# Kernel tuning notes

Hardware: AMD Instinct MI355X
Metric: run time of the kernel (lower is better)

## Reference

```python
import jax, jax.numpy as jnp
import numpy as np

D_MODEL = 1024
NHEAD = 16
HEAD_DIM = D_MODEL // NHEAD
B, T = 2, 2048


def setup_inputs() -> dict:
    key = jax.random.key(0)
    ks = jax.random.split(key, 11)
    s = 1.0 / np.sqrt(D_MODEL)
    inp = {
        'q': jax.random.normal(ks[0], (B, T, D_MODEL), jnp.float32),
        'k': jax.random.normal(ks[1], (B, T, D_MODEL), jnp.float32),
        'v': jax.random.normal(ks[2], (B, T, D_MODEL), jnp.float32),
        'Wq': jax.random.normal(ks[3], (D_MODEL, D_MODEL), jnp.float32) * s,
        'bq': jnp.zeros((D_MODEL,), jnp.float32),
        'Wk': jax.random.normal(ks[4], (D_MODEL, D_MODEL), jnp.float32) * s,
        'bk': jnp.zeros((D_MODEL,), jnp.float32),
        'Wv': jax.random.normal(ks[5], (D_MODEL, D_MODEL), jnp.float32) * s,
        'bv': jnp.zeros((D_MODEL,), jnp.float32),
        'Wo': jax.random.normal(ks[6], (D_MODEL, D_MODEL), jnp.float32) * s,
        'bo': jnp.zeros((D_MODEL,), jnp.float32),
    }
    return inp


def reference(q, k, v, Wq, bq, Wk, bk, Wv, bv, Wo, bo):
    scale = np.sqrt(HEAD_DIM).astype(np.float32)
    # projections (torch Linear: x @ W.T + b), split heads -> [B, H, T, Dh]
    def proj(x, W, b):
        y = jnp.einsum('btd,ed->bte', x, W) + b
        return y.reshape(B, T, NHEAD, HEAD_DIM).transpose(0, 2, 1, 3)
    qh = proj(q, Wq, bq)
    kh = proj(k, Wk, bk)
    vh = proj(v, Wv, bv)
    scores = jnp.einsum('bhqd,bhkd->bhqk', qh, kh) / scale  # [B,H,T,T]
    weights = jax.nn.softmax(scores, axis=-1)
    out = jnp.einsum('bhqk,bhkd->bhqd', weights, vh)        # [B,H,T,Dh]
    out = out.transpose(0, 2, 1, 3).reshape(B, T, D_MODEL)
    return jnp.einsum('btd,ed->bte', out, Wo) + bo
```

## Files before the change

### kernel.cpp

```cpp
#include <hip/hip_runtime.h>
#include <cstdint>
#include <cstddef>


#define D_MODEL 1024
#define NHEAD   16
#define HDIM    64
#define BATCH   2
#define SEQ     2048
#define BT      (BATCH * SEQ)

#define QSCALE 0.18033688011112043f

typedef __bf16 bf16;
typedef __bf16 bf16x8 __attribute__((ext_vector_type(8)));
typedef __bf16 bf16x4 __attribute__((ext_vector_type(4)));
typedef float  floatx4 __attribute__((ext_vector_type(4)));
typedef short  short4v __attribute__((ext_vector_type(4)));

#define MFMA16(a, b, c) __builtin_amdgcn_mfma_f32_16x16x32_bf16((a), (b), (c), 0, 0, 0)

__device__ __forceinline__ floatx4 MFMA16B(bf16x4 a, bf16x4 b, floatx4 c) {
  return __builtin_amdgcn_mfma_f32_16x16x16bf16_1k(
      __builtin_bit_cast(short4v, a), __builtin_bit_cast(short4v, b), c, 0, 0, 0);
}

__device__ __forceinline__ float fexp2(float x) {
  return __builtin_amdgcn_exp2f(x);
}

__device__ __forceinline__ void async_cp16(const bf16* g, bf16* l) {
  __builtin_amdgcn_global_load_lds(
      (__attribute__((address_space(1))) void*)(g),
      (__attribute__((address_space(3))) void*)(l), 16, 0, 0);
}

__global__ __launch_bounds__(256) void cvt7(
    const float* __restrict__ s0, const float* __restrict__ s1,
    const float* __restrict__ s2, const float* __restrict__ s3,
    const float* __restrict__ s4, const float* __restrict__ s5,
    const float* __restrict__ s6,
    bf16* __restrict__ d0, bf16* __restrict__ d1, bf16* __restrict__ d2,
    bf16* __restrict__ d3, bf16* __restrict__ d4, bf16* __restrict__ d5,
    bf16* __restrict__ d6)
{
  const float* src; bf16* dst; int n4;
  switch (blockIdx.y) {
    case 0:  src = s0; dst = d0; n4 = (BT * D_MODEL) / 4; break;
    case 1:  src = s1; dst = d1; n4 = (BT * D_MODEL) / 4; break;
    case 2:  src = s2; dst = d2; n4 = (BT * D_MODEL) / 4; break;
    case 3:  src = s3; dst = d3; n4 = (D_MODEL * D_MODEL) / 4; break;
    case 4:  src = s4; dst = d4; n4 = (D_MODEL * D_MODEL) / 4; break;
    case 5:  src = s5; dst = d5; n4 = (D_MODEL * D_MODEL) / 4; break;
    default: src = s6; dst = d6; n4 = (D_MODEL * D_MODEL) / 4; break;
  }
  int stride = gridDim.x * blockDim.x;
  for (int i = blockIdx.x * blockDim.x + threadIdx.x; i < n4; i += stride) {
    float4 f = ((const float4*)src)[i];
    bf16x4 h;
    h[0] = (bf16)f.x; h[1] = (bf16)f.y; h[2] = (bf16)f.z; h[3] = (bf16)f.w;
    ((bf16x4*)dst)[i] = h;
  }
}

__device__ __forceinline__ void gemm128_core(
    const bf16* __restrict__ A, const bf16* __restrict__ W,
    int m0, int n0, bf16* As, bf16* Bs, floatx4 acc[4][4])
{
  const int t = threadIdx.x;
  const int l = t & 63, w = t >> 6;
  const int quad = l >> 4, lr = l & 15;
  const int wm = (w >> 1) * 64, wn = (w & 1) * 64;

  floatx4 z = {0.f, 0.f, 0.f, 0.f};
#pragma unroll
  for (int i = 0; i < 4; i++)
#pragma unroll
    for (int j = 0; j < 4; j++) acc[i][j] = z;

  for (int kt = 0; kt < 1024; kt += 32) {
    __syncthreads();
#pragma unroll
    for (int i = 0; i < 2; i++) {
      int c = i * 256 + t;
      int row = c >> 2, ci = c & 3;
      async_cp16(A + (size_t)(m0 + row) * 1024 + kt + ci * 8,
                 As + (i * 256 + w * 64) * 8);
      async_cp16(W + (size_t)(n0 + row) * 1024 + kt + ci * 8,
                 Bs + (i * 256 + w * 64) * 8);
    }
    __syncthreads();

    bf16x8 af[4], bfr[4];
#pragma unroll
    for (int i = 0; i < 4; i++) {
      af[i]  = *(const bf16x8*)(As + (wm + i * 16 + lr) * 32 + quad * 8);
      bfr[i] = *(const bf16x8*)(Bs + (wn + i * 16 + lr) * 32 + quad * 8);
    }
#pragma unroll
    for (int i = 0; i < 4; i++)
#pragma unroll
      for (int j = 0; j < 4; j++)
        acc[i][j] = MFMA16(af[i], bfr[j], acc[i][j]);
  }
}

__global__ __launch_bounds__(256) void qkv_gemm(
    const bf16* __restrict__ qb, const bf16* __restrict__ kb, const bf16* __restrict__ vb,
    const bf16* __restrict__ wq, const bf16* __restrict__ wk, const bf16* __restrict__ wv,
    const float* __restrict__ biasq, const float* __restrict__ biask, const float* __restrict__ biasv,
    bf16* __restrict__ qh, bf16* __restrict__ kh, bf16* __restrict__ vt)
{
  __shared__ bf16 As[128 * 32];
  __shared__ bf16 Bs[128 * 32];
  const int zid = blockIdx.z;
  const bf16* A = (zid == 0) ? qb : ((zid == 1) ? kb : vb);
  const bf16* W = (zid == 0) ? wq : ((zid == 1) ? wk : wv);
  const float* bias = (zid == 0) ? biasq : ((zid == 1) ? biask : biasv);
  const int m0 = blockIdx.x * 128, n0 = blockIdx.y * 128;

  floatx4 acc[4][4];
  gemm128_core(A, W, m0, n0, As, Bs, acc);

  const int t = threadIdx.x, l = t & 63, w = t >> 6;
  const int quad = l >> 4, lr = l & 15;
  const int wm = (w >> 1) * 64, wn = (w & 1) * 64;
  const float sc = (zid == 0) ? QSCALE : 1.0f;

  if (zid < 2) {
    bf16* out = (zid == 0) ? qh : kh;
#pragma unroll
    for (int i = 0; i < 4; i++) {
      int mbase = m0 + wm + i * 16 + quad * 4;
      int b  = mbase >> 11;
      int tq = mbase & 2047;
#pragma unroll
      for (int j = 0; j < 4; j++) {
        int n = n0 + wn + j * 16 + lr;
        float bv = bias[n];
        int h = n >> 6, dh = n & 63;
        bf16* p = out + ((size_t)((b * NHEAD + h) * SEQ + tq)) * HDIM + dh;
#pragma unroll
        for (int r = 0; r < 4; r++)
          p[(size_t)r * HDIM] = (bf16)((acc[i][j][r] + bv) * sc);
      }
    }
  } else {
#pragma unroll
    for (int i = 0; i < 4; i++) {
      int mbase = m0 + wm + i * 16 + quad * 4;
      int b  = mbase >> 11;
      int tq = mbase & 2047;
#pragma unroll
      for (int j = 0; j < 4; j++) {
        int n = n0 + wn + j * 16 + lr;
        float bv = bias[n];
        int h = n >> 6, dh = n & 63;
        bf16x4 pk;
#pragma unroll
        for (int r = 0; r < 4; r++) pk[r] = (bf16)(acc[i][j][r] + bv);
        *(bf16x4*)(vt + ((size_t)((b * NHEAD + h) * HDIM + dh)) * SEQ + tq) = pk;
      }
    }
  }
}

__global__ __launch_bounds__(512, 4) void attn_fused(
    const bf16* __restrict__ qh, const bf16* __restrict__ kh,
    const bf16* __restrict__ vt, bf16* __restrict__ attn)
{
  __shared__ __align__(16) char smem[65536];

  const int t = threadIdx.x, l = t & 63, w = t >> 6;
  const int quad = l >> 4, lr = l & 15;
  const int bh = blockIdx.y;
  const int qt0 = blockIdx.x * 128;
  const bf16* qg = qh + (size_t)bh * SEQ * HDIM;
  const bf16* kg = kh + (size_t)bh * SEQ * HDIM;
  const bf16* vg = vt + (size_t)bh * HDIM * SEQ;

  int krow0 = (w * 2) * 8 + (l >> 3);
  int krow1 = (w * 2 + 1) * 8 + (l >> 3);
  int kcl0  = (l & 7) ^ (krow0 & 7);
  int kcl1  = (l & 7) ^ (krow1 & 7);
  int vrow0 = (w * 2) * 4 + (l >> 4);
  int vrow1 = (w * 2 + 1) * 4 + (l >> 4);
  int vcl0  = (l & 15) ^ (vrow0 & 15);
  int vcl1  = (l & 15) ^ (vrow1 & 15);
  const bf16* kga = kg + (size_t)krow0 * HDIM + kcl0 * 8;
  const bf16* kgb = kg + (size_t)krow1 * HDIM + kcl1 * 8;
  const bf16* vga = vg + (size_t)vrow0 * SEQ + vcl0 * 8;
  const bf16* vgb = vg + (size_t)vrow1 * SEQ + vcl1 * 8;

  bf16x8 qf[2];
#pragma unroll
  for (int ko = 0; ko < 2; ko++)
    qf[ko] = *(const bf16x8*)(qg + (size_t)(qt0 + w * 16 + lr) * HDIM
                              + ko * 32 + quad * 8);

  floatx4 zz = {0.f, 0.f, 0.f, 0.f};
  floatx4 Oacc[4];
#pragma unroll
  for (int dt = 0; dt < 4; dt++) Oacc[dt] = zz;
  float mrow = -3.0e38f, lrow = 0.f;

  {
    bf16* Kb = (bf16*)smem;
    bf16* Vb = (bf16*)(smem + 16384);
    async_cp16(kga, Kb + (w * 2) * 512);
    async_cp16(kgb, Kb + (w * 2 + 1) * 512);
    async_cp16(vga, Vb + (w * 2) * 512);
    async_cp16(vgb, Vb + (w * 2 + 1) * 512);
  }

  for (int kt = 0; kt < 16; kt++) {
    const int p = kt & 1;
    __syncthreads();
    if (kt + 1 < 16) {
      bf16* Kb = (bf16*)(smem + (1 - p) * 32768);
      bf16* Vb = (bf16*)(smem + (1 - p) * 32768 + 16384);
      int off = (kt + 1) * 128;
      async_cp16(kga + (size_t)off * HDIM, Kb + (w * 2) * 512);
      async_cp16(kgb + (size_t)off * HDIM, Kb + (w * 2 + 1) * 512);
      async_cp16(vga + off, Vb + (w * 2) * 512);
      async_cp16(vgb + off, Vb + (w * 2 + 1) * 512);
    }
    const bf16* Ks  = (const bf16*)(smem + p * 32768);
    const bf16* Vts = (const bf16*)(smem + p * 32768 + 16384);

    floatx4 s[8];
#pragma unroll
    for (int ni = 0; ni < 8; ni++) {
      const bf16* krow = Ks + (ni * 16 + lr) * 64;
      bf16x8 k0 = *(const bf16x8*)(krow + ((quad ^ (lr & 7)) * 8));
      bf16x8 k1 = *(const bf16x8*)(krow + (((quad + 4) ^ (lr & 7)) * 8));
      floatx4 a = zz;
      a = MFMA16(k0, qf[0], a);
      a = MFMA16(k1, qf[1], a);
      s[ni] = a;
    }

    float rmax = s[0][0];
#pragma unroll
    for (int ni = 0; ni < 8; ni++)
#pragma unroll
      for (int r = 0; r < 4; r++) rmax = fmaxf(rmax, s[ni][r]);
    rmax = fmaxf(rmax, __shfl_xor(rmax, 16, 64));
    rmax = fmaxf(rmax, __shfl_xor(rmax, 32, 64));
    float mnew = fmaxf(mrow, rmax);
    float al = fexp2(mrow - mnew);
    mrow = mnew;

    bf16x4 pk[8];
    float rsum = 0.f;
#pragma unroll
    for (int ni = 0; ni < 8; ni++)
#pragma unroll
      for (int r = 0; r < 4; r++) {
        float pv = fexp2(s[ni][r] - mnew);
        rsum += pv;
        pk[ni][r] = (bf16)pv;
      }
    rsum += __shfl_xor(rsum, 16, 64);
    rsum += __shfl_xor(rsum, 32, 64);
    lrow = lrow * al + rsum;
#pragma unroll
    for (int dt = 0; dt < 4; dt++)
#pragma unroll
      for (int r = 0; r < 4; r++) Oacc[dt][r] *= al;

#pragma unroll
    for (int ni = 0; ni < 8; ni++)
#pragma unroll
      for (int dt = 0; dt < 4; dt++) {
        bf16x4 vf = *(const bf16x4*)(Vts + (dt * 16 + lr) * 128
                                     + (((ni * 2 + (quad >> 1)) ^ lr) * 8)
                                     + (quad & 1) * 4);
        Oacc[dt] = MFMA16B(vf, pk[ni], Oacc[dt]);
      }
  }

  float inv = 1.0f / lrow;
  bf16* Ost = (bf16*)smem;
#pragma unroll
  for (int dt = 0; dt < 4; dt++) {
    bf16x4 ov;
#pragma unroll
    for (int r = 0; r < 4; r++) ov[r] = (bf16)(Oacc[dt][r] * inv);
    *(bf16x4*)(Ost + (size_t)(w * 16 + lr) * 72 + dt * 16 + quad * 4) = ov;
  }
  __syncthreads();

  const int b = bh >> 4, h = bh & 15;
#pragma unroll
  for (int i = 0; i < 2; i++) {
    int c = t + 512 * i;
    int row = c >> 3, ci = c & 7;
    *(int4*)(attn + ((size_t)b * SEQ + qt0 + row) * D_MODEL + h * HDIM + ci * 8) =
        *(const int4*)(Ost + row * 72 + ci * 8);
  }
}

__global__ __launch_bounds__(256) void oproj_gemm(
    const bf16* __restrict__ attn, const bf16* __restrict__ wo,
    const float* __restrict__ bo, float* __restrict__ out)
{
  __shared__ bf16 As[64 * 32];
  __shared__ bf16 Bs[64 * 32];
  const int m0 = blockIdx.x * 64, n0 = blockIdx.y * 64;
  const int t = threadIdx.x, l = t & 63, w = t >> 6;
  const int quad = l >> 4, lr = l & 15;
  const int wm = (w >> 1) * 32, wn = (w & 1) * 32;

  floatx4 z = {0.f, 0.f, 0.f, 0.f};
  floatx4 acc[2][2];
#pragma unroll
  for (int i = 0; i < 2; i++)
#pragma unroll
    for (int j = 0; j < 2; j++) acc[i][j] = z;

  for (int kt = 0; kt < 1024; kt += 32) {
    __syncthreads();
    {
      int row = t >> 2, ci = t & 3;
      async_cp16(attn + (size_t)(m0 + row) * 1024 + kt + ci * 8,
                 As + (w * 64) * 8);
      async_cp16(wo + (size_t)(n0 + row) * 1024 + kt + ci * 8,
                 Bs + (w * 64) * 8);
    }
    __syncthreads();

    bf16x8 af[2], bfr[2];
#pragma unroll
    for (int i = 0; i < 2; i++) {
      af[i]  = *(const bf16x8*)(As + (wm + i * 16 + lr) * 32 + quad * 8);
      bfr[i] = *(const bf16x8*)(Bs + (wn + i * 16 + lr) * 32 + quad * 8);
    }
#pragma unroll
    for (int i = 0; i < 2; i++)
#pragma unroll
      for (int j = 0; j < 2; j++)
        acc[i][j] = MFMA16(af[i], bfr[j], acc[i][j]);
  }

#pragma unroll
  for (int i = 0; i < 2; i++) {
    int m = m0 + wm + i * 16 + quad * 4;
#pragma unroll
    for (int j = 0; j < 2; j++) {
      int n = n0 + wn + j * 16 + lr;
      float bv = bo[n];
      float* p = out + (size_t)m * D_MODEL + n;
#pragma unroll
      for (int r = 0; r < 4; r++)
        p[(size_t)r * D_MODEL] = acc[i][j][r] + bv;
    }
  }
}

extern "C" void kernel_launch(void* const* d_in, const int* in_sizes, int n_in,
                              void* d_out, int out_size, void* d_ws, size_t ws_size,
                              hipStream_t stream)
{
  const float* q  = (const float*)d_in[0];
  const float* k  = (const float*)d_in[1];
  const float* v  = (const float*)d_in[2];
  const float* Wq = (const float*)d_in[3];
  const float* bq = (const float*)d_in[4];
  const float* Wk = (const float*)d_in[5];
  const float* bk = (const float*)d_in[6];
  const float* Wv = (const float*)d_in[7];
  const float* bv = (const float*)d_in[8];
  const float* Wo = (const float*)d_in[9];
  const float* bo = (const float*)d_in[10];

  const size_t NQ = (size_t)BT * D_MODEL;
  const size_t NW = (size_t)D_MODEL * D_MODEL;

  bf16* p = (bf16*)d_ws;
  bf16* qb   = p; p += NQ;
  bf16* kb   = p; p += NQ;
  bf16* vb   = p; p += NQ;
  bf16* wqb  = p; p += NW;
  bf16* wkb  = p; p += NW;
  bf16* wvb  = p; p += NW;
  bf16* wob  = p; p += NW;
  bf16* qhp  = p; p += NQ;
  bf16* khp  = p; p += NQ;
  bf16* vtp  = p; p += NQ;
  bf16* attn = p; p += NQ;

  cvt7<<<dim3(1024, 7, 1), 256, 0, stream>>>(q, k, v, Wq, Wk, Wv, Wo,
                                             qb, kb, vb, wqb, wkb, wvb, wob);
  qkv_gemm<<<dim3(32, 8, 3), 256, 0, stream>>>(qb, kb, vb, wqb, wkb, wvb,
                                               bq, bk, bv, qhp, khp, vtp);
  attn_fused<<<dim3(16, 32, 1), 512, 0, stream>>>(qhp, khp, vtp, attn);
  oproj_gemm<<<dim3(64, 16, 1), 256, 0, stream>>>(attn, wob, bo, (float*)d_out);
}
```

Baseline: 230.7 us.

## Process two query groups per wave in attention and skip small max rescales

The attention kernel now uses 4 waves of 256 threads instead of 8. Each wave handles 32 query rows as two 16-row groups, so every K and V fragment read from LDS feeds two MFMAs. This halves LDS traffic per unit of work and doubles per-wave registers. It also adds a lazy-rescale threshold: the running max and accumulators are updated only when some lane's new max exceeds the old by more than 8 (log2 units). This saves exp and multiply work, but the unnormalized values can grow up to 2^8 before rescaling.

```diff
diff --git a/kernel.cpp b/kernel.cpp
--- a/kernel.cpp
+++ b/kernel.cpp
@@ -165,7 +165,7 @@
   }
 }
 
-__global__ __launch_bounds__(512, 4) void attn_fused(
+__global__ __launch_bounds__(256, 2) void attn_fused(
     const bf16* __restrict__ qh, const bf16* __restrict__ kh,
     const bf16* __restrict__ vt, bf16* __restrict__ attn)
 {
@@ -179,122 +179,138 @@
   const bf16* kg = kh + (size_t)bh * SEQ * HDIM;
   const bf16* vg = vt + (size_t)bh * HDIM * SEQ;
 
-  int krow0 = (w * 2) * 8 + (l >> 3);
-  int krow1 = (w * 2 + 1) * 8 + (l >> 3);
-  int kcl0  = (l & 7) ^ (krow0 & 7);
-  int kcl1  = (l & 7) ^ (krow1 & 7);
-  int vrow0 = (w * 2) * 4 + (l >> 4);
-  int vrow1 = (w * 2 + 1) * 4 + (l >> 4);
-  int vcl0  = (l & 15) ^ (vrow0 & 15);
-  int vcl1  = (l & 15) ^ (vrow1 & 15);
-  const bf16* kga = kg + (size_t)krow0 * HDIM + kcl0 * 8;
-  const bf16* kgb = kg + (size_t)krow1 * HDIM + kcl1 * 8;
-  const bf16* vga = vg + (size_t)vrow0 * SEQ + vcl0 * 8;
-  const bf16* vgb = vg + (size_t)vrow1 * SEQ + vcl1 * 8;
-
-  bf16x8 qf[2];
-#pragma unroll
-  for (int ko = 0; ko < 2; ko++)
-    qf[ko] = *(const bf16x8*)(qg + (size_t)(qt0 + w * 16 + lr) * HDIM
-                              + ko * 32 + quad * 8);
-
-  floatx4 zz = {0.f, 0.f, 0.f, 0.f};
-  floatx4 Oacc[4];
-#pragma unroll
-  for (int dt = 0; dt < 4; dt++) Oacc[dt] = zz;
-  float mrow = -3.0e38f, lrow = 0.f;
-
-  {
-    bf16* Kb = (bf16*)smem;
-    bf16* Vb = (bf16*)(smem + 16384);
-    async_cp16(kga, Kb + (w * 2) * 512);
-    async_cp16(kgb, Kb + (w * 2 + 1) * 512);
-    async_cp16(vga, Vb + (w * 2) * 512);
-    async_cp16(vgb, Vb + (w * 2 + 1) * 512);
-  }
+  const bf16* kseg[4];
+  const bf16* vseg[4];
+#pragma unroll
+  for (int i = 0; i < 4; i++) {
+    int s = w * 4 + i;
+    int krow = s * 8 + (l >> 3);
+    kseg[i] = kg + (size_t)krow * HDIM + (((l & 7) ^ (l >> 3)) * 8);
+    int vrow = s * 4 + (l >> 4);
+    vseg[i] = vg + (size_t)vrow * SEQ + (((l & 15) ^ (vrow & 15)) * 8);
+  }
+
+  bf16x8 qf[2][2];
+#pragma unroll
+  for (int g = 0; g < 2; g++)
+#pragma unroll
+    for (int ko = 0; ko < 2; ko++)
+      qf[g][ko] = *(const bf16x8*)(qg + (size_t)(qt0 + w * 32 + g * 16 + lr) * HDIM
+                                   + ko * 32 + quad * 8);
+
+  const floatx4 zz = {0.f, 0.f, 0.f, 0.f};
+  floatx4 Oacc[2][4];
+#pragma unroll
+  for (int g = 0; g < 2; g++)
+#pragma unroll
+    for (int dt = 0; dt < 4; dt++) Oacc[g][dt] = zz;
+  float mrow[2] = {-3.0e38f, -3.0e38f};
+  float lrow[2] = {0.f, 0.f};
+
+  auto stage = [&](int buf, int kt) {
+    bf16* Kb = (bf16*)(smem + buf * 32768);
+    bf16* Vb = (bf16*)(smem + buf * 32768 + 16384);
+    int off = kt * 128;
+#pragma unroll
+    for (int i = 0; i < 4; i++) {
+      async_cp16(kseg[i] + (size_t)off * HDIM, Kb + (w * 4 + i) * 512);
+      async_cp16(vseg[i] + off,                Vb + (w * 4 + i) * 512);
+    }
+  };
+
+  stage(0, 0);
 
   for (int kt = 0; kt < 16; kt++) {
     const int p = kt & 1;
     __syncthreads();
-    if (kt + 1 < 16) {
-      bf16* Kb = (bf16*)(smem + (1 - p) * 32768);
-      bf16* Vb = (bf16*)(smem + (1 - p) * 32768 + 16384);
-      int off = (kt + 1) * 128;
-      async_cp16(kga + (size_t)off * HDIM, Kb + (w * 2) * 512);
-      async_cp16(kgb + (size_t)off * HDIM, Kb + (w * 2 + 1) * 512);
-      async_cp16(vga + off, Vb + (w * 2) * 512);
-      async_cp16(vgb + off, Vb + (w * 2 + 1) * 512);
-    }
+    if (kt + 1 < 16) stage(1 - p, kt + 1);
     const bf16* Ks  = (const bf16*)(smem + p * 32768);
     const bf16* Vts = (const bf16*)(smem + p * 32768 + 16384);
 
-    floatx4 s[8];
+    const bf16* krow0 = Ks + lr * 64 + ((quad ^ (lr & 7)) * 8);
+    const bf16* krow1 = Ks + lr * 64 + (((quad + 4) ^ (lr & 7)) * 8);
+
+    floatx4 s0[8], s1[8];
 #pragma unroll
     for (int ni = 0; ni < 8; ni++) {
-      const bf16* krow = Ks + (ni * 16 + lr) * 64;
-      bf16x8 k0 = *(const bf16x8*)(krow + ((quad ^ (lr & 7)) * 8));
-      bf16x8 k1 = *(const bf16x8*)(krow + (((quad + 4) ^ (lr & 7)) * 8));
-      floatx4 a = zz;
-      a = MFMA16(k0, qf[0], a);
-      a = MFMA16(k1, qf[1], a);
-      s[ni] = a;
-    }
-
-    float rmax = s[0][0];
-#pragma unroll
-    for (int ni = 0; ni < 8; ni++)
-#pragma unroll
-      for (int r = 0; r < 4; r++) rmax = fmaxf(rmax, s[ni][r]);
-    rmax = fmaxf(rmax, __shfl_xor(rmax, 16, 64));
-    rmax = fmaxf(rmax, __shfl_xor(rmax, 32, 64));
-    float mnew = fmaxf(mrow, rmax);
-    float al = fexp2(mrow - mnew);
-    mrow = mnew;
-
-    bf16x4 pk[8];
-    float rsum = 0.f;
-#pragma unroll
-    for (int ni = 0; ni < 8; ni++)
-#pragma unroll
-      for (int r = 0; r < 4; r++) {
-        float pv = fexp2(s[ni][r] - mnew);
-        rsum += pv;
-        pk[ni][r] = (bf16)pv;
+      bf16x8 k0 = *(const bf16x8*)(krow0 + ni * 1024);
+      bf16x8 k1 = *(const bf16x8*)(krow1 + ni * 1024);
+      floatx4 a0 = MFMA16(k0, qf[0][0], zz);
+      a0 = MFMA16(k1, qf[0][1], a0);
+      floatx4 a1 = MFMA16(k0, qf[1][0], zz);
+      a1 = MFMA16(k1, qf[1][1], a1);
+      s0[ni] = a0;
+      s1[ni] = a1;
+    }
+
+    bf16x4 pk0[8], pk1[8];
+#pragma unroll
+    for (int g = 0; g < 2; g++) {
+      floatx4* sg = g ? s1 : s0;
+      bf16x4* pkg = g ? pk1 : pk0;
+      float rmax = sg[0][0];
+#pragma unroll
+      for (int ni = 0; ni < 8; ni++)
+#pragma unroll
+        for (int r = 0; r < 4; r++) rmax = fmaxf(rmax, sg[ni][r]);
+      rmax = fmaxf(rmax, __shfl_xor(rmax, 16, 64));
+      rmax = fmaxf(rmax, __shfl_xor(rmax, 32, 64));
+      if (!__all(rmax - mrow[g] <= 8.0f)) {
+        float mnew = fmaxf(mrow[g], rmax);
+        float al = fexp2(mrow[g] - mnew);
+        mrow[g] = mnew;
+        lrow[g] *= al;
+#pragma unroll
+        for (int dt = 0; dt < 4; dt++)
+#pragma unroll
+          for (int r = 0; r < 4; r++) Oacc[g][dt][r] *= al;
       }
-    rsum += __shfl_xor(rsum, 16, 64);
-    rsum += __shfl_xor(rsum, 32, 64);
-    lrow = lrow * al + rsum;
-#pragma unroll
-    for (int dt = 0; dt < 4; dt++)
-#pragma unroll
-      for (int r = 0; r < 4; r++) Oacc[dt][r] *= al;
-
-#pragma unroll
-    for (int ni = 0; ni < 8; ni++)
+      float m = mrow[g];
+      float rsum = 0.f;
+#pragma unroll
+      for (int ni = 0; ni < 8; ni++)
+#pragma unroll
+        for (int r = 0; r < 4; r++) {
+          float pv = fexp2(sg[ni][r] - m);
+          rsum += pv;
+          pkg[ni][r] = (bf16)pv;
+        }
+      rsum += __shfl_xor(rsum, 16, 64);
+      rsum += __shfl_xor(rsum, 32, 64);
+      lrow[g] += rsum;
+    }
+
+    const bf16* vbase = Vts + lr * 128 + (quad & 1) * 4;
+#pragma unroll
+    for (int ni = 0; ni < 8; ni++) {
+      const bf16* vp = vbase + (((ni * 2 + (quad >> 1)) ^ lr) * 8);
 #pragma unroll
       for (int dt = 0; dt < 4; dt++) {
-        bf16x4 vf = *(const bf16x4*)(Vts + (dt * 16 + lr) * 128
-                                     + (((ni * 2 + (quad >> 1)) ^ lr) * 8)
-                                     + (quad & 1) * 4);
-        Oacc[dt] = MFMA16B(vf, pk[ni], Oacc[dt]);
+        bf16x4 vf = *(const bf16x4*)(vp + dt * 2048);
+        Oacc[0][dt] = MFMA16B(vf, pk0[ni], Oacc[0][dt]);
+        Oacc[1][dt] = MFMA16B(vf, pk1[ni], Oacc[1][dt]);
       }
-  }
-
-  float inv = 1.0f / lrow;
+    }
+  }
+
   bf16* Ost = (bf16*)smem;
 #pragma unroll
-  for (int dt = 0; dt < 4; dt++) {
-    bf16x4 ov;
-#pragma unroll
-    for (int r = 0; r < 4; r++) ov[r] = (bf16)(Oacc[dt][r] * inv);
-    *(bf16x4*)(Ost + (size_t)(w * 16 + lr) * 72 + dt * 16 + quad * 4) = ov;
+  for (int g = 0; g < 2; g++) {
+    float inv = 1.0f / lrow[g];
+#pragma unroll
+    for (int dt = 0; dt < 4; dt++) {
+      bf16x4 ov;
+#pragma unroll
+      for (int r = 0; r < 4; r++) ov[r] = (bf16)(Oacc[g][dt][r] * inv);
+      *(bf16x4*)(Ost + (size_t)(w * 32 + g * 16 + lr) * 72 + dt * 16 + quad * 4) = ov;
+    }
   }
   __syncthreads();
 
   const int b = bh >> 4, h = bh & 15;
 #pragma unroll
-  for (int i = 0; i < 2; i++) {
-    int c = t + 512 * i;
+  for (int i = 0; i < 4; i++) {
+    int c = t + 256 * i;
     int row = c >> 3, ci = c & 7;
     *(int4*)(attn + ((size_t)b * SEQ + qt0 + row) * D_MODEL + h * HDIM + ci * 8) =
         *(const int4*)(Ost + row * 72 + ci * 8);
@@ -394,6 +410,6 @@
                                              qb, kb, vb, wqb, wkb, wvb, wob);
   qkv_gemm<<<dim3(32, 8, 3), 256, 0, stream>>>(qb, kb, vb, wqb, wkb, wvb,
                                                bq, bk, bv, qhp, khp, vtp);
-  attn_fused<<<dim3(16, 32, 1), 512, 0, stream>>>(qhp, khp, vtp, attn);
+  attn_fused<<<dim3(16, 32, 1), 256, 0, stream>>>(qhp, khp, vtp, attn);
   oproj_gemm<<<dim3(64, 16, 1), 256, 0, stream>>>(attn, wob, bo, (float*)d_out);
 }
```

Result: faster. 223.6 us (-3.1%).
